# Performance work log

Measured on AMD Instinct MI355X. Metric: run time of the kernel, lower is better.

The kernel has to match this reference:

```python
import jax, jax.numpy as jnp
import numpy as np

EPS = 1e-12  # torch F.normalize eps

def _l2norm(x):
    n = jnp.linalg.norm(x, axis=-1, keepdims=True)
    return x / jnp.maximum(n, EPS)

def _encode(h, mask, W, b):
    # h: [B,S,H], mask: [B,S] int
    h = h * mask[..., None].astype(h.dtype)      # zero padded tokens
    pooled = h[:, 0]                             # pooling_type='cls'
    col = h[:, 1:] @ W + b                       # colbert_linear on tokens 1:
    return _l2norm(pooled), _l2norm(col)         # normalize=True


def setup_inputs() -> dict:
    key = jax.random.key(0)
    k1, k2, k3, k4, k5, k6 = jax.random.split(key, 6)
    Q, Sq, C, Sc, H, D = 64, 32, 256, 256, 768, 128
    return {
        "q_hidden": jax.random.normal(k1, (Q, Sq, H), jnp.float32),
        "c_hidden": jax.random.normal(k2, (C, Sc, H), jnp.float32),
        "W": jax.random.normal(k3, (H, D), jnp.float32) / np.sqrt(H).astype(np.float32),
        "b": jax.random.normal(k4, (D,), jnp.float32) * 0.01,
        "q_mask": jax.random.randint(k5, (Q, Sq), 0, 2, jnp.int32),
        "c_mask": jax.random.randint(k6, (C, Sc), 0, 2, jnp.int32),
    }


def reference(q_hidden, c_hidden, W, b, q_mask, c_mask):
    q_pooled, q_col = _encode(q_hidden, q_mask, W, b)   # q_col: [Q, Sq-1, D]
    c_pooled, c_col = _encode(c_hidden, c_mask, W, b)   # c_col: [C, Sc-1, D]
    # MaxSim late interaction (get_batch_colbert_sim)
    token_sim = jnp.einsum('qin,cjn->qicj', q_col, c_col)  # [Q, Sq-1, C, Sc-1]
    sim = token_sim.max(axis=-1)                           # max over doc tokens j
    denom = q_mask[:, 1:].sum(-1, keepdims=True).astype(sim.dtype)
    sim = sim.sum(axis=1) / denom                          # [Q, C]
    return sim, q_pooled, c_pooled
```

## Files before the change

### kernel.cpp

```cpp
#include <hip/hip_runtime.h>
#include <hip/hip_bf16.h>

#define QN 64
#define SQ 32
#define CN 256
#define SC 256
#define HD 768
#define DD 128

typedef __attribute__((ext_vector_type(8))) short short8;
typedef __attribute__((ext_vector_type(4))) float f32x4;

static __device__ __forceinline__ unsigned short f2bf(float x) {
  unsigned u = __float_as_uint(x);
  unsigned r = 0x7FFFu + ((u >> 16) & 1u);
  return (unsigned short)((u + r) >> 16);
}
static __device__ __forceinline__ unsigned pack2(float a, float b) {
  return (unsigned)f2bf(a) | ((unsigned)f2bf(b) << 16);
}

__global__ __launch_bounds__(256) void prep_kernel(
    const float* __restrict__ W,
    const float* __restrict__ qh, const int* __restrict__ qm,
    const float* __restrict__ ch, const int* __restrict__ cm,
    unsigned short* __restrict__ Wt,
    float* __restrict__ outq, float* __restrict__ outc,
    unsigned short* __restrict__ qcolP) {
  __shared__ float red[4];
  int bid = blockIdx.x, tid = threadIdx.x;

  if (bid < DD) {
    for (int k = tid; k < HD; k += 256)
      Wt[bid * HD + k] = f2bf(W[(size_t)k * DD + bid]);
    return;
  }

  int row = bid - DD;
  const float* src;
  float* dst;
  float m;
  if (row < QN) {
    src = qh + (size_t)row * SQ * HD;
    m = (float)qm[row * SQ];
    dst = outq + (size_t)row * HD;
  } else {
    int b = row - QN;
    src = ch + (size_t)b * SC * HD;
    m = (float)cm[b * SC];
    dst = outc + (size_t)b * HD;
  }
  float ss = 0.f;
  for (int k = tid; k < HD; k += 256) {
    float v = src[k] * m;
    ss += v * v;
  }
  int lane = tid & 63, wv = tid >> 6;
  for (int off = 32; off; off >>= 1) ss += __shfl_xor(ss, off);
  if (lane == 0) red[wv] = ss;
  __syncthreads();
  float tot = red[0] + red[1] + red[2] + red[3];
  float inv = 1.f / fmaxf(sqrtf(tot), 1e-12f);
  for (int k = tid; k < HD; k += 256) dst[k] = src[k] * m * inv;
  if (row < QN && tid < 64)
    ((unsigned*)(qcolP + ((size_t)row * 32 + 31) * DD))[tid] = 0u;
}

union ProjLDS {
  struct { unsigned short a[64 * 64]; unsigned short b[128 * 64]; } s;
  float c[64 * 132];
};

__global__ __launch_bounds__(256) void proj_kernel(
    const float* __restrict__ q_hidden, const float* __restrict__ c_hidden,
    const int* __restrict__ q_mask, const int* __restrict__ c_mask,
    const unsigned short* __restrict__ Wt, const float* __restrict__ bias,
    unsigned short* __restrict__ qcol, unsigned short* __restrict__ ccol) {
  __shared__ ProjLDS u;
  int bx = blockIdx.x;
  int isQ = (bx >= 1020) ? 1 : 0;
  int base = isQ ? (bx - 1020) : bx;
  const float* hidden = isQ ? q_hidden : c_hidden;
  const int* mask = isQ ? q_mask : c_mask;
  int S = isQ ? SQ : SC;
  int T = S - 1;
  int OUTS = isQ ? 32 : 256;
  unsigned short* out = isQ ? qcol : ccol;

  int tid = threadIdx.x, lane = tid & 63, w = tid >> 6;
  int lm = lane & 15, lq = lane >> 4;
  int wm = w & 1, wn = w >> 1;

  int ar = tid >> 2, aseg = tid & 3;
  int ag = base * 64 + ar;
  int ab = ag / T, at = ag - ab * T;
  const float* hrow = hidden + ((size_t)ab * S + at + 1) * HD + aseg * 16;
  float am = (float)mask[ab * S + at + 1];
  int bd = tid >> 1, bh = tid & 1;
  const unsigned short* wrow = Wt + (size_t)bd * HD + bh * 32;

  f32x4 acc[2][4];
#pragma unroll
  for (int i = 0; i < 2; ++i)
#pragma unroll
    for (int j = 0; j < 4; ++j) acc[i][j] = (f32x4){0.f, 0.f, 0.f, 0.f};

  float4 va[4];
  uint4 vb[4];
#pragma unroll
  for (int j = 0; j < 4; ++j) va[j] = ((const float4*)hrow)[j];
#pragma unroll
  for (int j = 0; j < 4; ++j) vb[j] = ((const uint4*)wrow)[j];

  for (int k0 = 0; k0 < HD; k0 += 64) {
    __syncthreads();
    {
      unsigned p[8];
      p[0] = pack2(va[0].x * am, va[0].y * am); p[1] = pack2(va[0].z * am, va[0].w * am);
      p[2] = pack2(va[1].x * am, va[1].y * am); p[3] = pack2(va[1].z * am, va[1].w * am);
      p[4] = pack2(va[2].x * am, va[2].y * am); p[5] = pack2(va[2].z * am, va[2].w * am);
      p[6] = pack2(va[3].x * am, va[3].y * am); p[7] = pack2(va[3].z * am, va[3].w * am);
      int kc0 = aseg * 2;
      int pk0 = kc0 ^ (ar & 7), pk1 = (kc0 + 1) ^ (ar & 7);
      *(uint4*)&u.s.a[(ar * 8 + pk0) * 8] = *(uint4*)&p[0];
      *(uint4*)&u.s.a[(ar * 8 + pk1) * 8] = *(uint4*)&p[4];
#pragma unroll
      for (int j = 0; j < 4; ++j) {
        int kc = bh * 4 + j;
        int pk = kc ^ (bd & 7);
        *(uint4*)&u.s.b[(bd * 8 + pk) * 8] = vb[j];
      }
    }
    __syncthreads();
    if (k0 + 64 < HD) {
      const float4* hp = (const float4*)(hrow + k0 + 64);
      const uint4* wp = (const uint4*)(wrow + k0 + 64);
#pragma unroll
      for (int j = 0; j < 4; ++j) va[j] = hp[j];
#pragma unroll
      for (int j = 0; j < 4; ++j) vb[j] = wp[j];
    }
#pragma unroll
    for (int kf = 0; kf < 2; ++kf) {
      short8 a2[2], b4[4];
#pragma unroll
      for (int mt = 0; mt < 2; ++mt) {
        int row = (wm * 2 + mt) * 16 + lm;
        int kc = kf * 4 + lq;
        a2[mt] = *(const short8*)&u.s.a[(row * 8 + (kc ^ (row & 7))) * 8];
      }
#pragma unroll
      for (int nt = 0; nt < 4; ++nt) {
        int row = (wn * 4 + nt) * 16 + lm;
        int kc = kf * 4 + lq;
        b4[nt] = *(const short8*)&u.s.b[(row * 8 + (kc ^ (row & 7))) * 8];
      }
#pragma unroll
      for (int mt = 0; mt < 2; ++mt)
#pragma unroll
        for (int nt = 0; nt < 4; ++nt)
          acc[mt][nt] = __builtin_amdgcn_mfma_f32_16x16x32_bf16(a2[mt], b4[nt], acc[mt][nt], 0, 0, 0);
    }
  }

  __syncthreads();
#pragma unroll
  for (int mt = 0; mt < 2; ++mt)
#pragma unroll
    for (int nt = 0; nt < 4; ++nt)
#pragma unroll
      for (int r = 0; r < 4; ++r) {
        int row = (wm * 2 + mt) * 16 + lq * 4 + r;
        int col = (wn * 4 + nt) * 16 + lm;
        u.c[row * 132 + col] = acc[mt][nt][r];
      }
  __syncthreads();

  int r2 = tid >> 2, seg2 = tid & 3;
  float v[32];
  float ss = 0.f;
#pragma unroll
  for (int j = 0; j < 8; ++j) {
    float4 cv = *(const float4*)&u.c[r2 * 132 + seg2 * 32 + j * 4];
    float4 bv = *(const float4*)&bias[seg2 * 32 + j * 4];
    v[4 * j + 0] = cv.x + bv.x; v[4 * j + 1] = cv.y + bv.y;
    v[4 * j + 2] = cv.z + bv.z; v[4 * j + 3] = cv.w + bv.w;
#pragma unroll
    for (int e = 0; e < 4; ++e) ss += v[4 * j + e] * v[4 * j + e];
  }
  ss += __shfl_xor(ss, 1);
  ss += __shfl_xor(ss, 2);
  float inv = 1.f / fmaxf(sqrtf(ss), 1e-12f);

  unsigned pk[16];
#pragma unroll
  for (int j = 0; j < 16; ++j) pk[j] = pack2(v[2 * j] * inv, v[2 * j + 1] * inv);

  int g = base * 64 + r2;
  int b = g / T, tt = g - b * T;
  unsigned short* dst = out + ((size_t)b * OUTS + tt) * DD + seg2 * 32;
  uint4* d4 = (uint4*)dst;
  d4[0] = *(uint4*)&pk[0];  d4[1] = *(uint4*)&pk[4];
  d4[2] = *(uint4*)&pk[8];  d4[3] = *(uint4*)&pk[12];
  if (!isQ && tt == 254) {
    uint4* d5 = (uint4*)(dst + DD);
    d5[0] = *(uint4*)&pk[0];  d5[1] = *(uint4*)&pk[4];
    d5[2] = *(uint4*)&pk[8];  d5[3] = *(uint4*)&pk[12];
  }
}

__global__ __launch_bounds__(128, 1) void sim_kernel(
    const unsigned short* __restrict__ qcolP,
    const unsigned short* __restrict__ ccol,
    const int* __restrict__ qmask,
    float* __restrict__ sim) {
  __shared__ unsigned short cbuf[256 * 128];
  int tid = threadIdx.x, lane = tid & 63, w = tid >> 6;
  int lm = lane & 15, lq = lane >> 4;
  int qb = blockIdx.y * 8 + w * 4;
  int c0 = blockIdx.x * 4;

  short8 af[4][2][4];
#pragma unroll
  for (int q2 = 0; q2 < 4; ++q2)
#pragma unroll
    for (int it = 0; it < 2; ++it)
#pragma unroll
      for (int kf = 0; kf < 4; ++kf)
        af[q2][it][kf] = *(const short8*)(qcolP +
            (((size_t)(qb + q2) * 32 + it * 16 + lm) * DD + kf * 32 + lq * 8));

  float dinv[4];
#pragma unroll
  for (int q2 = 0; q2 < 4; ++q2) {
    float v = (lane >= 1 && lane < 32) ? (float)qmask[(qb + q2) * SQ + lane] : 0.f;
    for (int off = 1; off < 64; off <<= 1) v += __shfl_xor(v, off);
    dinv[q2] = 1.f / v;
  }

  for (int cc = 0; cc < 4; ++cc) {
    int c = c0 + cc;
    __syncthreads();
    const uint4* src = (const uint4*)(ccol + (size_t)c * SC * DD);
#pragma unroll
    for (int g4 = 0; g4 < 4; ++g4) {
      uint4 tmp[8];
#pragma unroll
      for (int it = 0; it < 8; ++it) tmp[it] = src[(g4 * 8 + it) * 128 + tid];
#pragma unroll
      for (int it = 0; it < 8; ++it) {
        int idx = (g4 * 8 + it) * 128 + tid;
        int row = idx >> 4, kc = idx & 15;
        int pkc = (kc & 8) | ((kc & 7) ^ (row & 7));
        *(uint4*)&cbuf[(row * 16 + pkc) * 8] = tmp[it];
      }
    }
    __syncthreads();

    float rmax[4][2];
#pragma unroll
    for (int q2 = 0; q2 < 4; ++q2) { rmax[q2][0] = -__builtin_inff(); rmax[q2][1] = -__builtin_inff(); }

    for (int jt = 0; jt < 16; ++jt) {
      short8 cf[4];
#pragma unroll
      for (int kf = 0; kf < 4; ++kf) {
        int row = jt * 16 + lm;
        int kc = kf * 4 + lq;
        int pkc = (kc & 8) | ((kc & 7) ^ (row & 7));
        cf[kf] = *(const short8*)&cbuf[(row * 16 + pkc) * 8];
      }
#pragma unroll
      for (int q2 = 0; q2 < 4; ++q2)
#pragma unroll
        for (int it = 0; it < 2; ++it) {
          f32x4 acc = (f32x4){0.f, 0.f, 0.f, 0.f};
#pragma unroll
          for (int kf = 0; kf < 4; ++kf)
            acc = __builtin_amdgcn_mfma_f32_16x16x32_bf16(cf[kf], af[q2][it][kf], acc, 0, 0, 0);
          float loc = fmaxf(fmaxf(acc[0], acc[1]), fmaxf(acc[2], acc[3]));
          rmax[q2][it] = fmaxf(rmax[q2][it], loc);
        }
    }

#pragma unroll
    for (int q2 = 0; q2 < 4; ++q2) {
      float m0 = rmax[q2][0], m1 = rmax[q2][1];
      m0 = fmaxf(m0, __shfl_xor(m0, 16)); m0 = fmaxf(m0, __shfl_xor(m0, 32));
      m1 = fmaxf(m1, __shfl_xor(m1, 16)); m1 = fmaxf(m1, __shfl_xor(m1, 32));
      float s = m0 + ((lm == 15) ? 0.f : m1);
      s += __shfl_xor(s, 1); s += __shfl_xor(s, 2);
      s += __shfl_xor(s, 4); s += __shfl_xor(s, 8);
      if (lane == 0) sim[(qb + q2) * CN + c] = s * dinv[q2];
    }
  }
}

extern "C" void kernel_launch(void* const* d_in, const int* in_sizes, int n_in,
                              void* d_out, int out_size, void* d_ws, size_t ws_size,
                              hipStream_t stream) {
  const float* q_hidden = (const float*)d_in[0];
  const float* c_hidden = (const float*)d_in[1];
  const float* W = (const float*)d_in[2];
  const float* bias = (const float*)d_in[3];
  const int* q_mask = (const int*)d_in[4];
  const int* c_mask = (const int*)d_in[5];

  float* out = (float*)d_out;
  float* sim = out;
  float* q_pooled = out + QN * CN;
  float* c_pooled = q_pooled + QN * HD;

  unsigned short* Wt    = (unsigned short*)d_ws;
  unsigned short* qcolP = (unsigned short*)((char*)d_ws + (256 << 10));
  unsigned short* ccol  = (unsigned short*)((char*)d_ws + (1 << 20));

  prep_kernel<<<DD + QN + CN, 256, 0, stream>>>(W, q_hidden, q_mask, c_hidden, c_mask,
                                                Wt, q_pooled, c_pooled, qcolP);
  proj_kernel<<<1051, 256, 0, stream>>>(q_hidden, c_hidden, q_mask, c_mask,
                                        Wt, bias, qcolP, ccol);
  sim_kernel<<<dim3(64, 8), 128, 0, stream>>>(qcolP, ccol, q_mask, sim);
}
```

Baseline: 428.5 us.

## Restructure projection and MaxSim kernels with direct global-to-LDS loads and pre-swizzled layouts

Prep now writes W transposed to bf16 in a pre-swizzled chunk layout. The projection kernel uses 128-row tiles with 128 output columns per wave, loads W through global_load_lds, and reads the hidden rows straight from global memory into registers. The mask multiply moves into the epilogue, and ccol is written already swizzled. Because ccol arrives swizzled, the sim kernel can copy it into LDS with global_load_lds and skip the register staging; it also now runs 4 waves per block with 2 queries per wave. The intent is to cut LDS staging overhead and raise occupancy, at the cost of uncoalesced, unpipelined hidden-state loads in the projection.

```diff
diff --git a/kernel.cpp b/kernel.cpp
--- a/kernel.cpp
+++ b/kernel.cpp
@@ -20,19 +20,36 @@
   return (unsigned)f2bf(a) | ((unsigned)f2bf(b) << 16);
 }
 
+typedef const __attribute__((address_space(1))) unsigned int* as1_u32p;
+typedef __attribute__((address_space(3))) unsigned int* as3_u32p;
+static __device__ __forceinline__ void gl_lds16(const void* g, void* l) {
+  __builtin_amdgcn_global_load_lds((as1_u32p)g, (as3_u32p)l, 16, 0, 0);
+}
+
 __global__ __launch_bounds__(256) void prep_kernel(
     const float* __restrict__ W,
     const float* __restrict__ qh, const int* __restrict__ qm,
     const float* __restrict__ ch, const int* __restrict__ cm,
-    unsigned short* __restrict__ Wt,
+    unsigned short* __restrict__ WtS,
     float* __restrict__ outq, float* __restrict__ outc,
     unsigned short* __restrict__ qcolP) {
   __shared__ float red[4];
   int bid = blockIdx.x, tid = threadIdx.x;
 
   if (bid < DD) {
-    for (int k = tid; k < HD; k += 256)
-      Wt[bid * HD + k] = f2bf(W[(size_t)k * DD + bid]);
+    int d = bid;
+    if (tid < 96) {
+      int kc = tid;
+      unsigned p[4];
+#pragma unroll
+      for (int e = 0; e < 4; ++e) {
+        float a = W[(size_t)(kc * 8 + 2 * e) * DD + d];
+        float b = W[(size_t)(kc * 8 + 2 * e + 1) * DD + d];
+        p[e] = pack2(a, b);
+      }
+      int kcp = (kc & ~7) | ((kc & 7) ^ (d & 7));
+      *(uint4*)&WtS[((size_t)d * 96 + kcp) * 8] = *(uint4*)p;
+    }
     return;
   }
 
@@ -67,99 +84,82 @@
 }
 
 union ProjLDS {
-  struct { unsigned short a[64 * 64]; unsigned short b[128 * 64]; } s;
-  float c[64 * 132];
+  unsigned short b[128 * 32 * 8];
+  float cep[128 * 132];
 };
 
-__global__ __launch_bounds__(256) void proj_kernel(
+__global__ __launch_bounds__(256, 2) void proj_kernel(
     const float* __restrict__ q_hidden, const float* __restrict__ c_hidden,
     const int* __restrict__ q_mask, const int* __restrict__ c_mask,
-    const unsigned short* __restrict__ Wt, const float* __restrict__ bias,
+    const unsigned short* __restrict__ WtS, const float* __restrict__ bias,
     unsigned short* __restrict__ qcol, unsigned short* __restrict__ ccol) {
   __shared__ ProjLDS u;
   int bx = blockIdx.x;
-  int isQ = (bx >= 1020) ? 1 : 0;
-  int base = isQ ? (bx - 1020) : bx;
-  const float* hidden = isQ ? q_hidden : c_hidden;
-  const int* mask = isQ ? q_mask : c_mask;
-  int S = isQ ? SQ : SC;
-  int T = S - 1;
-  int OUTS = isQ ? 32 : 256;
-  unsigned short* out = isQ ? qcol : ccol;
-
-  int tid = threadIdx.x, lane = tid & 63, w = tid >> 6;
+  int isQ = (bx >= 510) ? 1 : 0;
+  int base = isQ ? (bx - 510) : bx;
+  int tid = threadIdx.x, lane = tid & 63, wv = tid >> 6;
   int lm = lane & 15, lq = lane >> 4;
-  int wm = w & 1, wn = w >> 1;
-
-  int ar = tid >> 2, aseg = tid & 3;
-  int ag = base * 64 + ar;
-  int ab = ag / T, at = ag - ab * T;
-  const float* hrow = hidden + ((size_t)ab * S + at + 1) * HD + aseg * 16;
-  float am = (float)mask[ab * S + at + 1];
-  int bd = tid >> 1, bh = tid & 1;
-  const unsigned short* wrow = Wt + (size_t)bd * HD + bh * 32;
-
-  f32x4 acc[2][4];
+
+  const float* hrow[2];
+#pragma unroll
+  for (int mt = 0; mt < 2; ++mt) {
+    int g = base * 128 + wv * 32 + mt * 16 + lm;
+    const float* hp;
+    if (isQ) {
+      g = (g < 1983) ? g : 1983;
+      int qq = g / 31, t = g - qq * 31;
+      hp = q_hidden + ((size_t)qq * SQ + t + 1) * HD;
+    } else {
+      int cb = g / 255, t = g - cb * 255;
+      hp = c_hidden + ((size_t)cb * SC + t + 1) * HD;
+    }
+    hrow[mt] = hp;
+  }
+
+  f32x4 acc[2][8];
 #pragma unroll
   for (int i = 0; i < 2; ++i)
 #pragma unroll
-    for (int j = 0; j < 4; ++j) acc[i][j] = (f32x4){0.f, 0.f, 0.f, 0.f};
-
-  float4 va[4];
-  uint4 vb[4];
-#pragma unroll
-  for (int j = 0; j < 4; ++j) va[j] = ((const float4*)hrow)[j];
-#pragma unroll
-  for (int j = 0; j < 4; ++j) vb[j] = ((const uint4*)wrow)[j];
-
-  for (int k0 = 0; k0 < HD; k0 += 64) {
+    for (int j = 0; j < 8; ++j) acc[i][j] = (f32x4){0.f, 0.f, 0.f, 0.f};
+
+  for (int stage = 0; stage < 3; ++stage) {
     __syncthreads();
-    {
-      unsigned p[8];
-      p[0] = pack2(va[0].x * am, va[0].y * am); p[1] = pack2(va[0].z * am, va[0].w * am);
-      p[2] = pack2(va[1].x * am, va[1].y * am); p[3] = pack2(va[1].z * am, va[1].w * am);
-      p[4] = pack2(va[2].x * am, va[2].y * am); p[5] = pack2(va[2].z * am, va[2].w * am);
-      p[6] = pack2(va[3].x * am, va[3].y * am); p[7] = pack2(va[3].z * am, va[3].w * am);
-      int kc0 = aseg * 2;
-      int pk0 = kc0 ^ (ar & 7), pk1 = (kc0 + 1) ^ (ar & 7);
-      *(uint4*)&u.s.a[(ar * 8 + pk0) * 8] = *(uint4*)&p[0];
-      *(uint4*)&u.s.a[(ar * 8 + pk1) * 8] = *(uint4*)&p[4];
-#pragma unroll
-      for (int j = 0; j < 4; ++j) {
-        int kc = bh * 4 + j;
-        int pk = kc ^ (bd & 7);
-        *(uint4*)&u.s.b[(bd * 8 + pk) * 8] = vb[j];
-      }
+#pragma unroll
+    for (int i = 0; i < 16; ++i) {
+      int d = i * 8 + wv * 2 + (lane >> 5);
+      int lc = lane & 31;
+      gl_lds16(WtS + ((size_t)d * 96 + stage * 32 + lc) * 8,
+               (char*)u.b + (size_t)(i * 256 + wv * 64) * 16);
     }
     __syncthreads();
-    if (k0 + 64 < HD) {
-      const float4* hp = (const float4*)(hrow + k0 + 64);
-      const uint4* wp = (const uint4*)(wrow + k0 + 64);
-#pragma unroll
-      for (int j = 0; j < 4; ++j) va[j] = hp[j];
-#pragma unroll
-      for (int j = 0; j < 4; ++j) vb[j] = wp[j];
-    }
-#pragma unroll
-    for (int kf = 0; kf < 2; ++kf) {
-      short8 a2[2], b4[4];
+
+#pragma unroll
+    for (int w = 0; w < 8; ++w) {
+      int kwin = stage * 8 + w;
+      short8 afr[2];
 #pragma unroll
       for (int mt = 0; mt < 2; ++mt) {
-        int row = (wm * 2 + mt) * 16 + lm;
-        int kc = kf * 4 + lq;
-        a2[mt] = *(const short8*)&u.s.a[(row * 8 + (kc ^ (row & 7))) * 8];
-      }
-#pragma unroll
-      for (int nt = 0; nt < 4; ++nt) {
-        int row = (wn * 4 + nt) * 16 + lm;
-        int kc = kf * 4 + lq;
-        b4[nt] = *(const short8*)&u.s.b[(row * 8 + (kc ^ (row & 7))) * 8];
+        const float* ha = hrow[mt] + kwin * 32 + lq * 8;
+        float4 a0 = *(const float4*)ha;
+        float4 a1 = *(const float4*)(ha + 4);
+        unsigned p[4];
+        p[0] = pack2(a0.x, a0.y); p[1] = pack2(a0.z, a0.w);
+        p[2] = pack2(a1.x, a1.y); p[3] = pack2(a1.z, a1.w);
+        afr[mt] = *(short8*)p;
+      }
+      int t = w * 4 + lq;
+      int lcp = (t & ~7) | ((t & 7) ^ (lm & 7));
+      short8 bfr[8];
+#pragma unroll
+      for (int nt = 0; nt < 8; ++nt) {
+        int ci = (nt * 16 + lm) * 32 + lcp;
+        bfr[nt] = *(const short8*)&u.b[(size_t)ci * 8];
       }
 #pragma unroll
       for (int mt = 0; mt < 2; ++mt)
 #pragma unroll
-        for (int nt = 0; nt < 4; ++nt)
-          acc[mt][nt] = __builtin_amdgcn_mfma_f32_16x16x32_bf16(a2[mt], b4[nt], acc[mt][nt], 0, 0, 0);
+        for (int nt = 0; nt < 8; ++nt)
+          acc[mt][nt] = __builtin_amdgcn_mfma_f32_16x16x32_bf16(afr[mt], bfr[nt], acc[mt][nt], 0, 0, 0);
     }
   }
 
@@ -167,62 +167,92 @@
 #pragma unroll
   for (int mt = 0; mt < 2; ++mt)
 #pragma unroll
-    for (int nt = 0; nt < 4; ++nt)
+    for (int nt = 0; nt < 8; ++nt)
 #pragma unroll
       for (int r = 0; r < 4; ++r) {
-        int row = (wm * 2 + mt) * 16 + lq * 4 + r;
-        int col = (wn * 4 + nt) * 16 + lm;
-        u.c[row * 132 + col] = acc[mt][nt][r];
+        int rw = wv * 32 + mt * 16 + lq * 4 + r;
+        int col = nt * 16 + lm;
+        u.cep[rw * 132 + col] = acc[mt][nt][r];
       }
   __syncthreads();
 
-  int r2 = tid >> 2, seg2 = tid & 3;
-  float v[32];
+  int tk = tid >> 1, hf = tid & 1;
+  int g = base * 128 + tk;
+  int qq, t, valid = 1;
+  float fm;
+  if (isQ) {
+    if (g >= 1983) { valid = (g == 1983); g = 1983; }
+    qq = g / 31; t = g - qq * 31;
+    fm = (float)q_mask[qq * SQ + t + 1];
+  } else {
+    qq = g / 255; t = g - qq * 255;
+    fm = (float)c_mask[qq * SC + t + 1];
+  }
+
+  float v[64];
   float ss = 0.f;
 #pragma unroll
+  for (int j = 0; j < 16; ++j) {
+    float4 cv = *(const float4*)&u.cep[tk * 132 + hf * 64 + j * 4];
+    float4 bv = *(const float4*)&bias[hf * 64 + j * 4];
+    v[4 * j + 0] = cv.x * fm + bv.x; v[4 * j + 1] = cv.y * fm + bv.y;
+    v[4 * j + 2] = cv.z * fm + bv.z; v[4 * j + 3] = cv.w * fm + bv.w;
+#pragma unroll
+    for (int e = 0; e < 4; ++e) ss += v[4 * j + e] * v[4 * j + e];
+  }
+  ss += __shfl_xor(ss, 1);
+  float inv = 1.f / fmaxf(sqrtf(ss), 1e-12f);
+
+  uint4 pk4[8];
+#pragma unroll
   for (int j = 0; j < 8; ++j) {
-    float4 cv = *(const float4*)&u.c[r2 * 132 + seg2 * 32 + j * 4];
-    float4 bv = *(const float4*)&bias[seg2 * 32 + j * 4];
-    v[4 * j + 0] = cv.x + bv.x; v[4 * j + 1] = cv.y + bv.y;
-    v[4 * j + 2] = cv.z + bv.z; v[4 * j + 3] = cv.w + bv.w;
-#pragma unroll
-    for (int e = 0; e < 4; ++e) ss += v[4 * j + e] * v[4 * j + e];
-  }
-  ss += __shfl_xor(ss, 1);
-  ss += __shfl_xor(ss, 2);
-  float inv = 1.f / fmaxf(sqrtf(ss), 1e-12f);
-
-  unsigned pk[16];
-#pragma unroll
-  for (int j = 0; j < 16; ++j) pk[j] = pack2(v[2 * j] * inv, v[2 * j + 1] * inv);
-
-  int g = base * 64 + r2;
-  int b = g / T, tt = g - b * T;
-  unsigned short* dst = out + ((size_t)b * OUTS + tt) * DD + seg2 * 32;
-  uint4* d4 = (uint4*)dst;
-  d4[0] = *(uint4*)&pk[0];  d4[1] = *(uint4*)&pk[4];
-  d4[2] = *(uint4*)&pk[8];  d4[3] = *(uint4*)&pk[12];
-  if (!isQ && tt == 254) {
-    uint4* d5 = (uint4*)(dst + DD);
-    d5[0] = *(uint4*)&pk[0];  d5[1] = *(uint4*)&pk[4];
-    d5[2] = *(uint4*)&pk[8];  d5[3] = *(uint4*)&pk[12];
-  }
-}
-
-__global__ __launch_bounds__(128, 1) void sim_kernel(
+    unsigned p[4];
+#pragma unroll
+    for (int e = 0; e < 4; ++e)
+      p[e] = pack2(v[8 * j + 2 * e] * inv, v[8 * j + 2 * e + 1] * inv);
+    pk4[j] = *(uint4*)p;
+  }
+
+  if (isQ) {
+    if (valid) {
+      uint4* dst = (uint4*)(qcol + ((size_t)qq * 32 + t) * DD + hf * 64);
+#pragma unroll
+      for (int j = 0; j < 8; ++j) dst[j] = pk4[j];
+    }
+  } else {
+    uint4* rowp = (uint4*)(ccol + ((size_t)qq * 256 + t) * DD);
+#pragma unroll
+    for (int j = 0; j < 8; ++j) {
+      int kc = hf * 8 + j;
+      int p = (kc & 8) | ((kc & 7) ^ (t & 7));
+      rowp[p] = pk4[j];
+    }
+    if (t == 254) {
+      uint4* rowp2 = rowp + 8;
+#pragma unroll
+      for (int j = 0; j < 8; ++j) {
+        int kc = hf * 8 + j;
+        int p = (kc & 8) | ((kc & 7) ^ 7);
+        rowp2[p] = pk4[j];
+      }
+    }
+  }
+}
+
+__global__ __launch_bounds__(256, 2) void sim_kernel(
     const unsigned short* __restrict__ qcolP,
     const unsigned short* __restrict__ ccol,
     const int* __restrict__ qmask,
     float* __restrict__ sim) {
   __shared__ unsigned short cbuf[256 * 128];
-  int tid = threadIdx.x, lane = tid & 63, w = tid >> 6;
+  int tid = threadIdx.x, lane = tid & 63, wv = tid >> 6;
   int lm = lane & 15, lq = lane >> 4;
-  int qb = blockIdx.y * 8 + w * 4;
+  int qb = blockIdx.y * 8 + wv * 2;
   int c0 = blockIdx.x * 4;
 
-  short8 af[4][2][4];
-#pragma unroll
-  for (int q2 = 0; q2 < 4; ++q2)
+  short8 af[2][2][4];
+#pragma unroll
+  for (int q2 = 0; q2 < 2; ++q2)
 #pragma unroll
     for (int it = 0; it < 2; ++it)
 #pragma unroll
@@ -230,9 +260,9 @@
         af[q2][it][kf] = *(const short8*)(qcolP +
             (((size_t)(qb + q2) * 32 + it * 16 + lm) * DD + kf * 32 + lq * 8));
 
-  float dinv[4];
-#pragma unroll
-  for (int q2 = 0; q2 < 4; ++q2) {
+  float dinv[2];
+#pragma unroll
+  for (int q2 = 0; q2 < 2; ++q2) {
     float v = (lane >= 1 && lane < 32) ? (float)qmask[(qb + q2) * SQ + lane] : 0.f;
     for (int off = 1; off < 64; off <<= 1) v += __shfl_xor(v, off);
     dinv[q2] = 1.f / v;
@@ -241,25 +271,17 @@
   for (int cc = 0; cc < 4; ++cc) {
     int c = c0 + cc;
     __syncthreads();
-    const uint4* src = (const uint4*)(ccol + (size_t)c * SC * DD);
-#pragma unroll
-    for (int g4 = 0; g4 < 4; ++g4) {
-      uint4 tmp[8];
-#pragma unroll
-      for (int it = 0; it < 8; ++it) tmp[it] = src[(g4 * 8 + it) * 128 + tid];
-#pragma unroll
-      for (int it = 0; it < 8; ++it) {
-        int idx = (g4 * 8 + it) * 128 + tid;
-        int row = idx >> 4, kc = idx & 15;
-        int pkc = (kc & 8) | ((kc & 7) ^ (row & 7));
-        *(uint4*)&cbuf[(row * 16 + pkc) * 8] = tmp[it];
-      }
+    const unsigned short* src = ccol + (size_t)c * SC * DD;
+#pragma unroll
+    for (int i = 0; i < 16; ++i) {
+      gl_lds16(src + (size_t)(i * 256 + wv * 64 + lane) * 8,
+               (char*)cbuf + (size_t)(i * 256 + wv * 64) * 16);
     }
     __syncthreads();
 
-    float rmax[4][2];
-#pragma unroll
-    for (int q2 = 0; q2 < 4; ++q2) { rmax[q2][0] = -__builtin_inff(); rmax[q2][1] = -__builtin_inff(); }
+    float rmax[2][2];
+#pragma unroll
+    for (int q2 = 0; q2 < 2; ++q2) { rmax[q2][0] = -__builtin_inff(); rmax[q2][1] = -__builtin_inff(); }
 
     for (int jt = 0; jt < 16; ++jt) {
       short8 cf[4];
@@ -267,11 +289,11 @@
       for (int kf = 0; kf < 4; ++kf) {
         int row = jt * 16 + lm;
         int kc = kf * 4 + lq;
-        int pkc = (kc & 8) | ((kc & 7) ^ (row & 7));
-        cf[kf] = *(const short8*)&cbuf[(row * 16 + pkc) * 8];
-      }
-#pragma unroll
-      for (int q2 = 0; q2 < 4; ++q2)
+        int p = (kc & 8) | ((kc & 7) ^ (row & 7));
+        cf[kf] = *(const short8*)&cbuf[(size_t)(row * 16 + p) * 8];
+      }
+#pragma unroll
+      for (int q2 = 0; q2 < 2; ++q2)
 #pragma unroll
         for (int it = 0; it < 2; ++it) {
           f32x4 acc = (f32x4){0.f, 0.f, 0.f, 0.f};
@@ -284,7 +306,7 @@
     }
 
 #pragma unroll
-    for (int q2 = 0; q2 < 4; ++q2) {
+    for (int q2 = 0; q2 < 2; ++q2) {
       float m0 = rmax[q2][0], m1 = rmax[q2][1];
       m0 = fmaxf(m0, __shfl_xor(m0, 16)); m0 = fmaxf(m0, __shfl_xor(m0, 32));
       m1 = fmaxf(m1, __shfl_xor(m1, 16)); m1 = fmaxf(m1, __shfl_xor(m1, 32));
@@ -311,13 +333,13 @@
   float* q_pooled = out + QN * CN;
   float* c_pooled = q_pooled + QN * HD;
 
-  unsigned short* Wt    = (unsigned short*)d_ws;
+  unsigned short* WtS   = (unsigned short*)d_ws;
   unsigned short* qcolP = (unsigned short*)((char*)d_ws + (256 << 10));
   unsigned short* ccol  = (unsigned short*)((char*)d_ws + (1 << 20));
 
   prep_kernel<<<DD + QN + CN, 256, 0, stream>>>(W, q_hidden, q_mask, c_hidden, c_mask,
-                                                Wt, q_pooled, c_pooled, qcolP);
-  proj_kernel<<<1051, 256, 0, stream>>>(q_hidden, c_hidden, q_mask, c_mask,
-                                        Wt, bias, qcolP, ccol);
-  sim_kernel<<<dim3(64, 8), 128, 0, stream>>>(qcolP, ccol, q_mask, sim);
-}
+                                                WtS, q_pooled, c_pooled, qcolP);
+  proj_kernel<<<526, 256, 0, stream>>>(q_hidden, c_hidden, q_mask, c_mask,
+                                       WtS, bias, qcolP, ccol);
+  sim_kernel<<<dim3(64, 8), 256, 0, stream>>>(qcolP, ccol, q_mask, sim);
+}
```

New measurement: 374.7 us. -12.6%, faster.
